# Kernel optimization log

Hardware: AMD Instinct MI355X
Metric: run time of the kernel (lower is better)

Reference implementation:

```python
import jax, jax.numpy as jnp
import numpy as np

V, E, H, L = 50257, 256, 1024, 2   # vocab, embed_dim, hidden_dim, num_layers
B, T, K = 64, 80, 5                # batch, max_len, top_k
TEMP = 0.75
TWO_PI_OVER_24 = np.float32(2.0 * np.pi / 24.0)


def setup_inputs() -> dict:
    key = jax.random.key(0)
    ks = jax.random.split(key, 12)
    n = lambda i, shape, s: (jax.random.normal(ks[i], shape, jnp.float32) * s)
    hours = jax.random.uniform(ks[0], (B,), jnp.float32) * 24.0
    return {
        "hours": hours,
        "tp_w1": n(1, (2, H), 0.5),
        "tp_b1": jnp.zeros((H,), jnp.float32),
        "tp_w2": n(2, (H, 2 * L * H), 0.02),
        "tp_b2": jnp.zeros((2 * L * H,), jnp.float32),
        "embed": n(3, (V, E), 0.1).at[0].set(0.0),  # padding_idx=0 row zeroed
        "w_ih0": n(4, (E, 4 * H), 0.05),
        "w_hh0": n(5, (H, 4 * H), 0.05),
        "b0": jnp.zeros((4 * H,), jnp.float32),     # b_ih + b_hh combined
        "w_ih1": n(6, (H, 4 * H), 0.05),
        "w_hh1": n(7, (H, 4 * H), 0.05),
        "b1": jnp.zeros((4 * H,), jnp.float32),
        "fc_w": n(8, (H, V), 0.02),
        "fc_b": jnp.zeros((V,), jnp.float32),
        "sos_id": 1,
    }


def _lstm_cell(x, h, c, w_ih, w_hh, b):
    # torch gate order: i, f, g, o
    g = x @ w_ih + h @ w_hh + b
    i, f, gg, o = jnp.split(g, 4, axis=-1)
    c2 = jax.nn.sigmoid(f) * c + jax.nn.sigmoid(i) * jnp.tanh(gg)
    h2 = jax.nn.sigmoid(o) * jnp.tanh(c2)
    return h2, c2


def reference(hours, tp_w1, tp_b1, tp_w2, tp_b2, embed,
              w_ih0, w_hh0, b0, w_ih1, w_hh1, b1, fc_w, fc_b, sos_id):
    # _encode_time: sin/cos of hour angle -> MLP -> (h0, c0) per layer
    a = hours * TWO_PI_OVER_24
    feat = jnp.stack([jnp.sin(a), jnp.cos(a)], axis=-1)          # [B,2]
    tp = jnp.tanh(feat @ tp_w1 + tp_b1) @ tp_w2 + tp_b2          # [B,2*L*H]
    tp = tp.reshape(B, L, 2, H)
    h = jnp.transpose(tp[:, :, 0, :], (1, 0, 2))                 # [L,B,H]
    c = jnp.transpose(tp[:, :, 1, :], (1, 0, 2))                 # [L,B,H]

    keys = jax.random.split(jax.random.key(42), T)

    def step(carry, k):
        h, c, tok = carry
        x = embed[tok]                                           # [B,E]
        h0n, c0n = _lstm_cell(x, h[0], c[0], w_ih0, w_hh0, b0)
        h1n, c1n = _lstm_cell(h0n, h[1], c[1], w_ih1, w_hh1, b1)
        logits = (h1n @ fc_w + fc_b) / TEMP                      # [B,V]
        topv, topi = jax.lax.top_k(logits, K)                    # [B,K]
        probs = jax.nn.softmax(topv, axis=-1)
        sel = jax.random.categorical(k, topv, axis=-1)           # [B], == multinomial(probs)
        nxt = jnp.take_along_axis(topi, sel[:, None], axis=1)[:, 0]
        return (jnp.stack([h0n, h1n]), jnp.stack([c0n, c1n]), nxt), (nxt, probs)

    tok0 = jnp.full((B,), sos_id, jnp.int32)
    _, (toks, probs) = jax.lax.scan(step, (h, c, tok0), keys)
    # toks: [T,B] -> [B,T]; probs: [T,B,K] -> [B,T,K]
    return jnp.transpose(toks, (1, 0)), jnp.transpose(probs, (1, 0, 2))
```

## Files before the change

### kernel.cpp

```cpp
#include <hip/hip_runtime.h>
#include <math.h>
#include <stdint.h>
#include <limits.h>

#define VSZ 50257
#define ESZ 256
#define HSZ 1024
#define BSZ 64
#define TSZ 80
#define GC  4096
#define NFCB 786
#define NCAND (NFCB*5)
#define NSLOT 26
#define NREF 12

typedef unsigned int u32;
typedef unsigned short u16;
typedef double f64x4 __attribute__((ext_vector_type(4)));
typedef float f32x4v __attribute__((ext_vector_type(4)));
typedef __bf16 bf16x8 __attribute__((ext_vector_type(8)));
union BFrag { u16 u[8]; bf16x8 v; };

__device__ __forceinline__ u16 f2bf(float f) {
  u32 x = __float_as_uint(f);
  return (u16)((x + 0x7FFFu + ((x >> 16) & 1u)) >> 16);
}
__device__ __forceinline__ float bf2f(u16 h) { return __uint_as_float(((u32)h) << 16); }

__device__ __forceinline__ void tf2x32(u32 k0, u32 k1, u32& x0, u32& x1) {
  u32 ks2 = k0 ^ k1 ^ 0x1BD11BDAu;
  x0 += k0; x1 += k1;
#define RND(r) { x0 += x1; x1 = (x1 << r) | (x1 >> (32 - r)); x1 ^= x0; }
  RND(13) RND(15) RND(26) RND(6)
  x0 += k1; x1 += ks2 + 1u;
  RND(17) RND(29) RND(16) RND(24)
  x0 += ks2; x1 += k0 + 2u;
  RND(13) RND(15) RND(26) RND(6)
  x0 += k0; x1 += k1 + 3u;
  RND(17) RND(29) RND(16) RND(24)
  x0 += k1; x1 += ks2 + 4u;
  RND(13) RND(15) RND(26) RND(6)
  x0 += ks2; x1 += k0 + 5u;
#undef RND
}

__device__ __forceinline__ double dsig(double x) { return 0.5 + 0.5 * tanh(0.5 * x); }

__device__ __forceinline__ void ins5(double v, int i, double* tv, int* ti) {
  bool beat4 = (v > tv[4]) || (v == tv[4] && i < ti[4]);
  if (!beat4) return;
  tv[4] = v; ti[4] = i;
#pragma unroll
  for (int p = 4; p > 0; --p) {
    bool sw = (tv[p] > tv[p-1]) || (tv[p] == tv[p-1] && ti[p] < ti[p-1]);
    double a0 = sw ? tv[p] : tv[p-1]; double a1 = sw ? tv[p-1] : tv[p];
    tv[p-1] = a0; tv[p] = a1;
    int b0 = sw ? ti[p] : ti[p-1]; int b1 = sw ? ti[p-1] : ti[p];
    ti[p-1] = b0; ti[p] = b1;
  }
}

__device__ __forceinline__ double dref(int m, int n) {
  int s = 0;
#pragma unroll
  for (int k = 0; k < 4; ++k) s += (4*m + k + 1) * (16*k + n + 1);
  return (double)s;
}

__global__ __launch_bounds__(64) void k_probe(int* __restrict__ fbp) {
  int l = threadIdx.x;
  int lane16 = l & 15, sub = l >> 4;
  {
    double av = (double)(4 * lane16 + sub + 1);
    double bv = (double)(16 * sub + lane16 + 1);
    f64x4 acc = {0., 0., 0., 0.};
    acc = __builtin_amdgcn_mfma_f64_16x16x4f64(av, bv, acc, 0, 0, 0);
    bool o0 = true, o1 = true, o2 = true, o3 = true;
#pragma unroll
    for (int j = 0; j < 4; ++j) {
      double d = acc[j];
      o0 = o0 && (d == dref(4 * sub + j, lane16));
      o1 = o1 && (d == dref(lane16, 4 * sub + j));
      o2 = o2 && (d == dref(sub + 4 * j, lane16));
      o3 = o3 && (d == dref(lane16, sub + 4 * j));
    }
    int a0 = __all(o0), a1 = __all(o1), a2 = __all(o2), a3 = __all(o3);
    if (l == 0) { fbp[0] = a0 ? 0 : a1 ? 1 : a2 ? 2 : 3; fbp[1] = 0; }
  }
  {
    BFrag fa, fbv;
#pragma unroll
    for (int i = 0; i < 8; ++i) {
      int k = sub * 8 + i;
      fa.u[i]  = f2bf((float)((lane16 * 5 + k * 3) % 63 + 1));
      fbv.u[i] = f2bf((float)((k * 7 + lane16 * 11) % 61 + 1));
    }
    f32x4v c = {0.f, 0.f, 0.f, 0.f};
    c = __builtin_amdgcn_mfma_f32_16x16x32_bf16(fa.v, fbv.v, c, 0, 0, 0);
    bool okb = true;
#pragma unroll
    for (int j = 0; j < 4; ++j) {
      int mm = sub * 4 + j, nn = lane16;
      int ref = 0;
      for (int k = 0; k < 32; ++k) ref += ((mm*5 + k*3) % 63 + 1) * ((k*7 + nn*11) % 61 + 1);
      okb = okb && (c[j] == (float)ref);
    }
    int allb = __all(okb);
    if (l == 0) fbp[2] = allb;
  }
}

__global__ __launch_bounds__(256) void k_rng(double* __restrict__ gum) {
  int idx = blockIdx.x * 256 + threadIdx.x;
  if (idx >= TSZ * 320) return;
  int t = idx / 320, m = idx % 320;
  u32 a0 = 0u, a1 = (u32)t;
  tf2x32(0u, 42u, a0, a1);
  u32 x0 = 0u, x1 = (u32)m;
  tf2x32(a0, a1, x0, x1);
  u32 bits = x0 ^ x1;
  const float TINY = 1.17549435082228750797e-38f;
  float f = __uint_as_float((bits >> 9) | 0x3f800000u) - 1.0f;
  float u = f + TINY;
  u = fmaxf(TINY, u);
  gum[idx] = -log(-log((double)u));
}

__global__ __launch_bounds__(256) void k_time1(const float* __restrict__ hours, const float* __restrict__ w1,
                                               const float* __restrict__ bb1, double* __restrict__ tp1T) {
  int idx = blockIdx.x * 256 + threadIdx.x;
  int b = idx & 63, hcol = idx >> 6;
  const float TPO = (float)(2.0 * 3.14159265358979323846 / 24.0);
  float af = hours[b] * TPO;
  double a = (double)af;
  double sv = sin(a), cv = cos(a);
  double vv = tanh(sv * (double)w1[hcol] + cv * (double)w1[HSZ + hcol] + (double)bb1[hcol]);
  tp1T[(size_t)hcol * 64 + b] = vv;
}

__global__ __launch_bounds__(256) void k_gemm_simple(const double* __restrict__ XTa, const float* __restrict__ Wa,
                                                     int Ka, int Sa, double* __restrict__ part) {
  int j = blockIdx.x * 256 + threadIdx.x;
  if (j >= GC) return;
  int s = blockIdx.y;
  int kc = Ka / Sa, k0 = s * kc;
  double acc[BSZ];
#pragma unroll
  for (int b = 0; b < BSZ; ++b) acc[b] = 0.0;
  const float* wp = Wa + (size_t)k0 * GC + j;
  const double* xp = XTa + (size_t)k0 * 64;
  for (int k = 0; k < kc; ++k) {
    double wv = (double)wp[0]; wp += GC;
#pragma unroll
    for (int b = 0; b < BSZ; ++b) acc[b] = fma(wv, xp[b], acc[b]);
    xp += 64;
  }
  double* o = part + ((size_t)s * 64) * GC + j;
#pragma unroll
  for (int b = 0; b < BSZ; ++b) o[(size_t)b * GC] = acc[b];
}

__global__ __launch_bounds__(256) void k_t2r(const double* __restrict__ part, const float* __restrict__ b2,
                                             double* __restrict__ h0T, double* __restrict__ c0,
                                             double* __restrict__ h1T, double* __restrict__ c1) {
  int b = blockIdx.y;
  int j = blockIdx.x * 256 + threadIdx.x;
  double acc = (double)b2[j];
  for (int s = 0; s < 8; ++s) acc += part[((size_t)s * 64 + b) * GC + j];
  int l = j >> 11, half = (j >> 10) & 1, hcol = j & 1023;
  if (half == 0) (l ? h1T : h0T)[(size_t)hcol * 64 + b] = acc;
  else           (l ? c1 : c0)[(size_t)b * HSZ + hcol] = acc;
}

__global__ __launch_bounds__(256, 4) void k_lstm_mfma(const double* __restrict__ x0, const float* __restrict__ W0,
                                                      const double* __restrict__ x1, const float* __restrict__ W1,
                                                      const double* __restrict__ x2, const float* __restrict__ W2,
                                                      int s1, int s2, double* __restrict__ part,
                                                      const int* __restrict__ fbp) {
  int conv = fbp[0] & 3;
  __shared__ double xs[64 * 64];
  int tid = threadIdx.x;
  int l = tid & 63, wv = tid >> 6;
  int sub = l >> 4, lane16 = l & 15;
  int colbase = blockIdx.x * 64;
  int s = blockIdx.y;
  const double* XT; const float* W; int k0;
  if (s < s1)      { XT = x0; W = W0; k0 = s * 128; }
  else if (s < s2) { XT = x1; W = W1; k0 = (s - s1) * 128; }
  else             { XT = x2; W = W2; k0 = (s - s2) * 128; }
  int colA = colbase + wv * 16 + lane16;
  f64x4 a0 = {0.,0.,0.,0.}, a1 = {0.,0.,0.,0.}, a2 = {0.,0.,0.,0.}, a3 = {0.,0.,0.,0.};
  const float* wp = W + (size_t)(k0 + sub) * GC + colA;
  float ab[8];
#pragma unroll
  for (int u = 0; u < 8; ++u) { ab[u] = wp[0]; wp += (size_t)4 * GC; }
  for (int ch = 0; ch < 2; ++ch) {
    __syncthreads();
    const double2* src = (const double2*)(XT + (size_t)(k0 + ch * 64) * 64);
    double2* dst = (double2*)xs;
    for (int i = tid; i < 2048; i += 256) dst[i] = src[i];
    __syncthreads();
#pragma unroll
    for (int g = 0; g < 2; ++g) {
#pragma unroll
      for (int u = 0; u < 8; ++u) {
        int ks = g * 8 + u;
        int step = ch * 16 + ks;
        float nv = 0.f;
        if (step + 8 < 32) nv = wp[0];
        wp += (size_t)4 * GC;
        double av = (double)ab[u];
        const double* bp = xs + (ks * 4 + sub) * 64 + lane16;
        double b0 = bp[0], b1 = bp[16], b2 = bp[32], b3 = bp[48];
        a0 = __builtin_amdgcn_mfma_f64_16x16x4f64(av, b0, a0, 0, 0, 0);
        a1 = __builtin_amdgcn_mfma_f64_16x16x4f64(av, b1, a1, 0, 0, 0);
        a2 = __builtin_amdgcn_mfma_f64_16x16x4f64(av, b2, a2, 0, 0, 0);
        a3 = __builtin_amdgcn_mfma_f64_16x16x4f64(av, b3, a3, 0, 0, 0);
        ab[u] = nv;
      }
    }
  }
#pragma unroll
  for (int j = 0; j < 4; ++j) {
    int m = (conv == 0) ? sub * 4 + j : (conv == 2) ? sub + 4 * j : lane16;
    int n = (conv == 0) ? lane16 : (conv == 2) ? lane16 : ((conv == 1) ? sub * 4 + j : sub + 4 * j);
    size_t base = ((size_t)s * 64 + n) * GC + colbase + wv * 16 + m;
    part[base]                   = a0[j];
    part[base + (size_t)16 * GC] = a1[j];
    part[base + (size_t)32 * GC] = a2[j];
    part[base + (size_t)48 * GC] = a3[j];
  }
}

__global__ __launch_bounds__(256) void k_cell(const double* __restrict__ part, int sBeg, int S,
                                              const float* __restrict__ bias,
                                              double* __restrict__ c, double* __restrict__ hT,
                                              int emit, u16* __restrict__ xh, u16* __restrict__ xl) {
  int b = blockIdx.y;
  int hcol = blockIdx.x * 256 + threadIdx.x;
  double gi = (double)bias[hcol];
  double gf = (double)bias[1024 + hcol];
  double gg = (double)bias[2048 + hcol];
  double go = (double)bias[3072 + hcol];
#pragma unroll 4
  for (int s = sBeg; s < sBeg + S; ++s) {
    const double* p = part + ((size_t)s * 64 + b) * GC;
    gi += p[hcol]; gf += p[1024 + hcol]; gg += p[2048 + hcol]; go += p[3072 + hcol];
  }
  size_t ci = (size_t)b * HSZ + hcol;
  double cn = dsig(gf) * c[ci] + dsig(gi) * tanh(gg);
  double hn = dsig(go) * tanh(cn);
  c[ci] = cn;
  hT[(size_t)hcol * 64 + b] = hn;
  if (emit) {
    u16 hb = f2bf((float)hn);
    double r = hn - (double)bf2f(hb);
    u16 lb = f2bf((float)r);
    size_t ti2 = (((size_t)(hcol >> 3)) * 64 + b) * 8 + (hcol & 7);
    xh[ti2] = hb;
    xl[ti2] = lb;
  }
}

__global__ __launch_bounds__(256, 4) void k_fcbf(const u16* __restrict__ xhg, const u16* __restrict__ xlg,
                                                 const float* __restrict__ W, const float* __restrict__ fcb,
                                                 double* __restrict__ candV, int* __restrict__ candI,
                                                 const int* __restrict__ fbp) {
  if (fbp[2] == 0) return;
  __shared__ double xs[64 * 64];
  u16* lx = (u16*)xs;
  int tid = threadIdx.x;
  int l = tid & 63, wv = tid >> 6;
  int sub = l >> 4, lane16 = l & 15;
  int vbase = blockIdx.x * 64;
  int colA = min(vbase + wv * 16 + lane16, VSZ - 1);
  f32x4v acc0 = {0,0,0,0}, acc1 = {0,0,0,0}, acc2 = {0,0,0,0}, acc3 = {0,0,0,0};
  for (int ch = 0; ch < 8; ++ch) {
    float wraw[32];
    const float* wb = W + (size_t)(ch * 128) * VSZ + colA;
#pragma unroll
    for (int q = 0; q < 32; ++q) {
      int k = ((q >> 3) * 32) + sub * 8 + (q & 7);
      wraw[q] = wb[(size_t)k * VSZ];
    }
    __syncthreads();
    {
      const uint4* sh = (const uint4*)(xhg + (size_t)ch * 8192);
      const uint4* sl = (const uint4*)(xlg + (size_t)ch * 8192);
      uint4* dh = (uint4*)lx;
      uint4* dl = (uint4*)(lx + 8192);
      for (int i = tid; i < 1024; i += 256) { dh[i] = sh[i]; dl[i] = sl[i]; }
    }
    __syncthreads();
#pragma unroll
    for (int kt = 0; kt < 4; ++kt) {
      BFrag wh, wl;
#pragma unroll
      for (int i = 0; i < 8; ++i) {
        float w = wraw[kt * 8 + i];
        u16 hb = f2bf(w);
        wh.u[i] = hb;
        wl.u[i] = f2bf(w - bf2f(hb));
      }
      int r = kt * 4 + sub;
#define BT_STEP(BT, ACC)                                                              \
      {                                                                               \
        int bb = BT * 16 + lane16;                                                    \
        bf16x8 xhv = *(const bf16x8*)(lx + (((size_t)r * 64 + bb) << 3));             \
        bf16x8 xlv = *(const bf16x8*)(lx + 8192 + (((size_t)r * 64 + bb) << 3));      \
        ACC = __builtin_amdgcn_mfma_f32_16x16x32_bf16(wh.v, xhv, ACC, 0, 0, 0);       \
        ACC = __builtin_amdgcn_mfma_f32_16x16x32_bf16(wh.v, xlv, ACC, 0, 0, 0);       \
        ACC = __builtin_amdgcn_mfma_f32_16x16x32_bf16(wl.v, xhv, ACC, 0, 0, 0);       \
      }
      BT_STEP(0, acc0)
      BT_STEP(1, acc1)
      BT_STEP(2, acc2)
      BT_STEP(3, acc3)
#undef BT_STEP
    }
  }
  __syncthreads();
#pragma unroll
  for (int j = 0; j < 4; ++j) {
    int vl = wv * 16 + sub * 4 + j;
    int v = vbase + vl;
    bool okv = (v < VSZ);
    double bi = okv ? (double)fcb[min(v, VSZ - 1)] : 0.0;
    int b0i = lane16, b1i = 16 + lane16, b2i = 32 + lane16, b3i = 48 + lane16;
    xs[b0i * 64 + ((vl + b0i) & 63)] = okv ? ((double)acc0[j] + bi) / 0.75 : -INFINITY;
    xs[b1i * 64 + ((vl + b1i) & 63)] = okv ? ((double)acc1[j] + bi) / 0.75 : -INFINITY;
    xs[b2i * 64 + ((vl + b2i) & 63)] = okv ? ((double)acc2[j] + bi) / 0.75 : -INFINITY;
    xs[b3i * 64 + ((vl + b3i) & 63)] = okv ? ((double)acc3[j] + bi) / 0.75 : -INFINITY;
  }
  __syncthreads();
  if (tid < 64) {
    int b = tid;
    double tv[5]; int ti[5];
#pragma unroll
    for (int p = 0; p < 5; ++p) { tv[p] = -INFINITY; ti[p] = INT_MAX; }
    for (int vl2 = 0; vl2 < 64; ++vl2)
      ins5(xs[b * 64 + ((vl2 + b) & 63)], vbase + vl2, tv, ti);
#pragma unroll
    for (int r = 0; r < 5; ++r) {
      candV[(size_t)b * NCAND + blockIdx.x * 5 + r] = tv[r];
      candI[(size_t)b * NCAND + blockIdx.x * 5 + r] = ti[r];
    }
  }
}

__global__ __launch_bounds__(256, 4) void k_fcf64(const double* __restrict__ h1T, const float* __restrict__ W,
                                                  const float* __restrict__ fcb,
                                                  double* __restrict__ candV, int* __restrict__ candI,
                                                  const int* __restrict__ fbp) {
  if (fbp[2] != 0) return;
  int conv = fbp[0] & 3;
  __shared__ double xs[64 * 64];
  int tid = threadIdx.x;
  int l = tid & 63, wv = tid >> 6;
  int sub = l >> 4, lane16 = l & 15;
  int vbase = blockIdx.x * 64;
  int colA = min(vbase + wv * 16 + lane16, VSZ - 1);
  f64x4 a0 = {0.,0.,0.,0.}, a1 = {0.,0.,0.,0.}, a2 = {0.,0.,0.,0.}, a3 = {0.,0.,0.,0.};
  const float* wp = W + (size_t)sub * VSZ + colA;
  float ab[8];
#pragma unroll
  for (int u = 0; u < 8; ++u) { ab[u] = wp[0]; wp += (size_t)4 * VSZ; }
  for (int ch = 0; ch < 16; ++ch) {
    __syncthreads();
    const double2* src = (const double2*)(h1T + (size_t)ch * 64 * 64);
    double2* dst = (double2*)xs;
    for (int i = tid; i < 2048; i += 256) dst[i] = src[i];
    __syncthreads();
#pragma unroll
    for (int g = 0; g < 2; ++g) {
#pragma unroll
      for (int u = 0; u < 8; ++u) {
        int ks = g * 8 + u;
        int step = ch * 16 + ks;
        float nv = 0.f;
        if (step + 8 < 256) nv = wp[0];
        wp += (size_t)4 * VSZ;
        double av = (double)ab[u];
        const double* bp = xs + (ks * 4 + sub) * 64 + lane16;
        double b0 = bp[0], b1 = bp[16], b2 = bp[32], b3 = bp[48];
        a0 = __builtin_amdgcn_mfma_f64_16x16x4f64(av, b0, a0, 0, 0, 0);
        a1 = __builtin_amdgcn_mfma_f64_16x16x4f64(av, b1, a1, 0, 0, 0);
        a2 = __builtin_amdgcn_mfma_f64_16x16x4f64(av, b2, a2, 0, 0, 0);
        a3 = __builtin_amdgcn_mfma_f64_16x16x4f64(av, b3, a3, 0, 0, 0);
        ab[u] = nv;
      }
    }
  }
  __syncthreads();
#pragma unroll
  for (int j = 0; j < 4; ++j) {
    int m = (conv == 0) ? sub * 4 + j : (conv == 2) ? sub + 4 * j : lane16;
    int n = (conv == 0) ? lane16 : (conv == 2) ? lane16 : ((conv == 1) ? sub * 4 + j : sub + 4 * j);
    int vl = wv * 16 + m;
    int v = vbase + vl;
    bool okv = (v < VSZ);
    double bi = okv ? (double)fcb[min(v, VSZ - 1)] : 0.0;
    int b0i = n, b1i = 16 + n, b2i = 32 + n, b3i = 48 + n;
    xs[b0i * 64 + ((vl + b0i) & 63)] = okv ? (a0[j] + bi) / 0.75 : -INFINITY;
    xs[b1i * 64 + ((vl + b1i) & 63)] = okv ? (a1[j] + bi) / 0.75 : -INFINITY;
    xs[b2i * 64 + ((vl + b2i) & 63)] = okv ? (a2[j] + bi) / 0.75 : -INFINITY;
    xs[b3i * 64 + ((vl + b3i) & 63)] = okv ? (a3[j] + bi) / 0.75 : -INFINITY;
  }
  __syncthreads();
  if (tid < 64) {
    int b = tid;
    double tv[5]; int ti[5];
#pragma unroll
    for (int p = 0; p < 5; ++p) { tv[p] = -INFINITY; ti[p] = INT_MAX; }
    for (int vl2 = 0; vl2 < 64; ++vl2)
      ins5(xs[b * 64 + ((vl2 + b) & 63)], vbase + vl2, tv, ti);
#pragma unroll
    for (int r = 0; r < 5; ++r) {
      candV[(size_t)b * NCAND + blockIdx.x * 5 + r] = tv[r];
      candI[(size_t)b * NCAND + blockIdx.x * 5 + r] = ti[r];
    }
  }
}

__global__ __launch_bounds__(256) void k_rfin(const double* __restrict__ candV, const int* __restrict__ candI,
                                              const float* __restrict__ W, const float* __restrict__ fcb,
                                              const double* __restrict__ h1T,
                                              const double* __restrict__ gum, int t,
                                              const float* __restrict__ embed,
                                              float* __restrict__ out, double* __restrict__ xt0) {
  __shared__ float sv[NCAND];
  __shared__ int   si[NCAND];
  __shared__ double redw[4];
  __shared__ float wvv[4]; __shared__ int wvi[4]; __shared__ int wvs[4];
  int b = blockIdx.x, tid = threadIdx.x;
  int l = tid & 63, wvd = tid >> 6;
  for (int e = tid; e < NCAND; e += 256) {
    sv[e] = (float)candV[(size_t)b * NCAND + e];
    si[e] = candI[(size_t)b * NCAND + e];
  }
  __syncthreads();
  int cidx[NREF];
#pragma unroll
  for (int r = 0; r < NREF; ++r) {
    float bv = -INFINITY; int bi = INT_MAX, bs = 0;
    for (int e = tid; e < NCAND; e += 256) {
      float v = sv[e]; int i2 = si[e];
      if (v > bv || (v == bv && i2 < bi)) { bv = v; bi = i2; bs = e; }
    }
#pragma unroll
    for (int off = 1; off < 64; off <<= 1) {
      float ov = __shfl_xor(bv, off, 64);
      int oi = __shfl_xor(bi, off, 64);
      int os = __shfl_xor(bs, off, 64);
      if (ov > bv || (ov == bv && oi < bi)) { bv = ov; bi = oi; bs = os; }
    }
    if (l == 0) { wvv[wvd] = bv; wvi[wvd] = bi; wvs[wvd] = bs; }
    __syncthreads();
    float fv = wvv[0]; int fi = wvi[0], fs = wvs[0];
#pragma unroll
    for (int q = 1; q < 4; ++q) {
      float ov = wvv[q]; int oi = wvi[q], os = wvs[q];
      if (ov > fv || (ov == fv && oi < fi)) { fv = ov; fi = oi; fs = os; }
    }
    cidx[r] = fi;
    __syncthreads();
    if (tid == 0) sv[fs] = -INFINITY;
    __syncthreads();
  }
  double ex[NREF];
#pragma unroll
  for (int c = 0; c < NREF; ++c) {
    int vc = cidx[c];
    double p = 0.0;
    for (int k = tid; k < HSZ; k += 256)
      p = fma((double)W[(size_t)k * VSZ + vc], h1T[(size_t)k * 64 + b], p);
#pragma unroll
    for (int off = 1; off < 64; off <<= 1) p += __shfl_xor(p, off, 64);
    if (l == 0) redw[wvd] = p;
    __syncthreads();
    ex[c] = ((redw[0] + redw[1] + redw[2] + redw[3]) + (double)fcb[vc]) / 0.75;
    __syncthreads();
  }
  double tv[5]; int ti[5];
#pragma unroll
  for (int p = 0; p < 5; ++p) { tv[p] = -INFINITY; ti[p] = INT_MAX; }
#pragma unroll
  for (int c = 0; c < NREF; ++c) ins5(ex[c], cidx[c], tv, ti);
  const double* g = gum + (size_t)t * 320 + b * 5;
  double bestv = tv[0] + g[0]; int best = 0;
#pragma unroll
  for (int k2 = 1; k2 < 5; ++k2) { double vv2 = tv[k2] + g[k2]; if (vv2 > bestv) { bestv = vv2; best = k2; } }
  int nxt = ti[best];
  if (tid == 0) {
    out[b * TSZ + t] = (float)nxt;
    double m = tv[0];
    double exx[5]; double s = 0.0;
#pragma unroll
    for (int k2 = 0; k2 < 5; ++k2) { exx[k2] = exp(tv[k2] - m); s += exx[k2]; }
    float* po = out + BSZ * TSZ + ((size_t)b * TSZ + t) * 5;
#pragma unroll
    for (int k2 = 0; k2 < 5; ++k2) po[k2] = (float)(exx[k2] / s);
  }
  xt0[(size_t)tid * 64 + b] = (double)embed[(size_t)nxt * ESZ + tid];
}

__global__ __launch_bounds__(256) void k_emb0(const float* __restrict__ embed, const int* __restrict__ sos,
                                              double* __restrict__ xt0) {
  int idx = blockIdx.x * 256 + threadIdx.x;
  int b = idx & 63, k = idx >> 6;
  xt0[(size_t)k * 64 + b] = (double)embed[(size_t)sos[0] * ESZ + k];
}

extern "C" void kernel_launch(void* const* d_in, const int* in_sizes, int n_in,
                              void* d_out, int out_size, void* d_ws, size_t ws_size,
                              hipStream_t stream) {
  const float* hours = (const float*)d_in[0];
  const float* tp_w1 = (const float*)d_in[1];
  const float* tp_b1 = (const float*)d_in[2];
  const float* tp_w2 = (const float*)d_in[3];
  const float* tp_b2 = (const float*)d_in[4];
  const float* embed = (const float*)d_in[5];
  const float* w_ih0 = (const float*)d_in[6];
  const float* w_hh0 = (const float*)d_in[7];
  const float* b0    = (const float*)d_in[8];
  const float* w_ih1 = (const float*)d_in[9];
  const float* w_hh1 = (const float*)d_in[10];
  const float* b1    = (const float*)d_in[11];
  const float* fc_w  = (const float*)d_in[12];
  const float* fc_b  = (const float*)d_in[13];
  const int*   sos   = (const int*)d_in[14];
  float* out = (float*)d_out;

  char* w = (char*)d_ws;
  double* part = (double*)w;  w += (size_t)NSLOT * 64 * GC * 8;
  double* xt0  = (double*)w;  w += (size_t)ESZ * 64 * 8;
  double* h0T  = (double*)w;  w += (size_t)HSZ * 64 * 8;
  double* h1T  = (double*)w;  w += (size_t)HSZ * 64 * 8;
  double* c0   = (double*)w;  w += (size_t)BSZ * HSZ * 8;
  double* c1   = (double*)w;  w += (size_t)BSZ * HSZ * 8;
  double* tp1T = (double*)w;  w += (size_t)HSZ * 64 * 8;
  double* gum  = (double*)w;  w += (size_t)TSZ * 320 * 8;
  double* candV = (double*)w; w += (size_t)BSZ * NCAND * 8;
  int*    candI = (int*)w;    w += (size_t)BSZ * NCAND * 4;
  int*    fbuf  = (int*)w;    w += 64;
  u16*    xhg   = (u16*)w;    w += (size_t)HSZ * 64 * 2;
  u16*    xlg   = (u16*)w;    w += (size_t)HSZ * 64 * 2;

  k_probe<<<dim3(1), dim3(64), 0, stream>>>(fbuf);
  k_rng<<<dim3(100), dim3(256), 0, stream>>>(gum);
  k_time1<<<dim3(256), dim3(256), 0, stream>>>(hours, tp_w1, tp_b1, tp1T);
  k_gemm_simple<<<dim3(16, 8), dim3(256), 0, stream>>>(tp1T, tp_w2, 1024, 8, part);
  k_t2r<<<dim3(16, 64), dim3(256), 0, stream>>>(part, tp_b2, h0T, c0, h1T, c1);
  k_emb0<<<dim3(64), dim3(256), 0, stream>>>(embed, sos, xt0);

  double* part18 = part + (size_t)18 * 64 * GC;
  for (int t = 0; t < TSZ; ++t) {
    k_lstm_mfma<<<dim3(64, 18), dim3(256), 0, stream>>>(xt0, w_ih0, h0T, w_hh0, h1T, w_hh1, 2, 10, part, fbuf);
    k_cell<<<dim3(4, 64), dim3(256), 0, stream>>>(part, 0, 10, b0, c0, h0T, 0, xhg, xlg);
    k_lstm_mfma<<<dim3(64, 8), dim3(256), 0, stream>>>(h0T, w_ih1, h0T, w_ih1, h0T, w_ih1, 8, 8, part18, fbuf);
    k_cell<<<dim3(4, 64), dim3(256), 0, stream>>>(part, 10, 16, b1, c1, h1T, 1, xhg, xlg);
    k_fcbf<<<dim3(NFCB), dim3(256), 0, stream>>>(xhg, xlg, fc_w, fc_b, candV, candI, fbuf);
    k_fcf64<<<dim3(NFCB), dim3(256), 0, stream>>>(h1T, fc_w, fc_b, candV, candI, fbuf);
    k_rfin<<<dim3(64), dim3(256), 0, stream>>>(candV, candI, fc_w, fc_b, h1T, gum, t, embed, out, xt0);
  }
}
```

Before: 20.50 ms.

## Pre-convert FC weights to transposed bf16 and drop split-bf16 candidate pass

Converts the fc weight matrix once per call into a transposed bf16 copy, so the per-step candidate GEMM loads contiguous bf16 rows and issues one MFMA per tile instead of three (hi/lo split). It also swizzles the shared-memory layout of the hidden state. The LSTM split-K slices grow from 128 to 256, which halves the partial-sum slots and launched blocks, and the top-candidate refinement count rises to 16 with one warp per candidate and no per-candidate barriers. This trades candidate accuracy for speed, covered by the larger exact-fp64 refinement set, and needs about 100MB of extra workspace, falling back to the fp64 path when that is not available.

```diff
diff --git a/kernel.cpp b/kernel.cpp
--- a/kernel.cpp
+++ b/kernel.cpp
@@ -11,8 +11,8 @@
 #define GC  4096
 #define NFCB 786
 #define NCAND (NFCB*5)
-#define NSLOT 26
-#define NREF 12
+#define NSLOT 13
+#define NREF 16
 
 typedef unsigned int u32;
 typedef unsigned short u16;
@@ -110,6 +110,25 @@
   }
 }
 
+__global__ __launch_bounds__(256) void k_wconv(const float* __restrict__ W, u16* __restrict__ whT) {
+  __shared__ u16 tile[64][65];
+  int vb = blockIdx.x * 64, kb = blockIdx.y * 64;
+  int tid = threadIdx.x;
+#pragma unroll
+  for (int i = 0; i < 16; ++i) {
+    int r = i * 4 + (tid >> 6), c = tid & 63;
+    int v = vb + c;
+    tile[c][r] = (v < VSZ) ? f2bf(W[(size_t)(kb + r) * VSZ + v]) : (u16)0;
+  }
+  __syncthreads();
+#pragma unroll
+  for (int i = 0; i < 16; ++i) {
+    int r = i * 4 + (tid >> 6), c = tid & 63;
+    int v = vb + r;
+    if (v < VSZ) whT[(size_t)v * 1024 + kb + c] = tile[r][c];
+  }
+}
+
 __global__ __launch_bounds__(256) void k_rng(double* __restrict__ gum) {
   int idx = blockIdx.x * 256 + threadIdx.x;
   if (idx >= TSZ * 320) return;
@@ -185,16 +204,16 @@
   int colbase = blockIdx.x * 64;
   int s = blockIdx.y;
   const double* XT; const float* W; int k0;
-  if (s < s1)      { XT = x0; W = W0; k0 = s * 128; }
-  else if (s < s2) { XT = x1; W = W1; k0 = (s - s1) * 128; }
-  else             { XT = x2; W = W2; k0 = (s - s2) * 128; }
+  if (s < s1)      { XT = x0; W = W0; k0 = s * 256; }
+  else if (s < s2) { XT = x1; W = W1; k0 = (s - s1) * 256; }
+  else             { XT = x2; W = W2; k0 = (s - s2) * 256; }
   int colA = colbase + wv * 16 + lane16;
   f64x4 a0 = {0.,0.,0.,0.}, a1 = {0.,0.,0.,0.}, a2 = {0.,0.,0.,0.}, a3 = {0.,0.,0.,0.};
   const float* wp = W + (size_t)(k0 + sub) * GC + colA;
   float ab[8];
 #pragma unroll
   for (int u = 0; u < 8; ++u) { ab[u] = wp[0]; wp += (size_t)4 * GC; }
-  for (int ch = 0; ch < 2; ++ch) {
+  for (int ch = 0; ch < 4; ++ch) {
     __syncthreads();
     const double2* src = (const double2*)(XT + (size_t)(k0 + ch * 64) * 64);
     double2* dst = (double2*)xs;
@@ -207,7 +226,7 @@
         int ks = g * 8 + u;
         int step = ch * 16 + ks;
         float nv = 0.f;
-        if (step + 8 < 32) nv = wp[0];
+        if (step + 8 < 64) nv = wp[0];
         wp += (size_t)4 * GC;
         double av = (double)ab[u];
         const double* bp = xs + (ks * 4 + sub) * 64 + lane16;
@@ -235,7 +254,7 @@
 __global__ __launch_bounds__(256) void k_cell(const double* __restrict__ part, int sBeg, int S,
                                               const float* __restrict__ bias,
                                               double* __restrict__ c, double* __restrict__ hT,
-                                              int emit, u16* __restrict__ xh, u16* __restrict__ xl) {
+                                              int emit, u16* __restrict__ xh) {
   int b = blockIdx.y;
   int hcol = blockIdx.x * 256 + threadIdx.x;
   double gi = (double)bias[hcol];
@@ -252,18 +271,12 @@
   double hn = dsig(go) * tanh(cn);
   c[ci] = cn;
   hT[(size_t)hcol * 64 + b] = hn;
-  if (emit) {
-    u16 hb = f2bf((float)hn);
-    double r = hn - (double)bf2f(hb);
-    u16 lb = f2bf((float)r);
-    size_t ti2 = (((size_t)(hcol >> 3)) * 64 + b) * 8 + (hcol & 7);
-    xh[ti2] = hb;
-    xl[ti2] = lb;
-  }
-}
-
-__global__ __launch_bounds__(256, 4) void k_fcbf(const u16* __restrict__ xhg, const u16* __restrict__ xlg,
-                                                 const float* __restrict__ W, const float* __restrict__ fcb,
+  if (emit)
+    xh[(size_t)(hcol >> 7) * 8192 + (size_t)b * 128 + (hcol & 127)] = f2bf((float)hn);
+}
+
+__global__ __launch_bounds__(256, 4) void k_fcbf(const u16* __restrict__ xhg, const u16* __restrict__ whT,
+                                                 const float* __restrict__ fcb,
                                                  double* __restrict__ candV, int* __restrict__ candI,
                                                  const int* __restrict__ fbp) {
   if (fbp[2] == 0) return;
@@ -274,44 +287,32 @@
   int sub = l >> 4, lane16 = l & 15;
   int vbase = blockIdx.x * 64;
   int colA = min(vbase + wv * 16 + lane16, VSZ - 1);
+  const u16* wrow = whT + (size_t)colA * 1024;
   f32x4v acc0 = {0,0,0,0}, acc1 = {0,0,0,0}, acc2 = {0,0,0,0}, acc3 = {0,0,0,0};
   for (int ch = 0; ch < 8; ++ch) {
-    float wraw[32];
-    const float* wb = W + (size_t)(ch * 128) * VSZ + colA;
-#pragma unroll
-    for (int q = 0; q < 32; ++q) {
-      int k = ((q >> 3) * 32) + sub * 8 + (q & 7);
-      wraw[q] = wb[(size_t)k * VSZ];
-    }
+    bf16x8 wh0 = *(const bf16x8*)(wrow + ch * 128 + 0 * 32 + sub * 8);
+    bf16x8 wh1 = *(const bf16x8*)(wrow + ch * 128 + 1 * 32 + sub * 8);
+    bf16x8 wh2 = *(const bf16x8*)(wrow + ch * 128 + 2 * 32 + sub * 8);
+    bf16x8 wh3 = *(const bf16x8*)(wrow + ch * 128 + 3 * 32 + sub * 8);
     __syncthreads();
     {
-      const uint4* sh = (const uint4*)(xhg + (size_t)ch * 8192);
-      const uint4* sl = (const uint4*)(xlg + (size_t)ch * 8192);
-      uint4* dh = (uint4*)lx;
-      uint4* dl = (uint4*)(lx + 8192);
-      for (int i = tid; i < 1024; i += 256) { dh[i] = sh[i]; dl[i] = sl[i]; }
+      const uint4* sg = (const uint4*)(xhg + (size_t)ch * 8192);
+      uint4* dl = (uint4*)lx;
+#pragma unroll
+      for (int i = 0; i < 4; ++i) {
+        int u = tid + i * 256;
+        int bswz = u >> 4, g = u & 15;
+        dl[(bswz << 4) | (g ^ (bswz & 7))] = sg[u];
+      }
     }
     __syncthreads();
 #pragma unroll
     for (int kt = 0; kt < 4; ++kt) {
-      BFrag wh, wl;
-#pragma unroll
-      for (int i = 0; i < 8; ++i) {
-        float w = wraw[kt * 8 + i];
-        u16 hb = f2bf(w);
-        wh.u[i] = hb;
-        wl.u[i] = f2bf(w - bf2f(hb));
-      }
-      int r = kt * 4 + sub;
-#define BT_STEP(BT, ACC)                                                              \
-      {                                                                               \
-        int bb = BT * 16 + lane16;                                                    \
-        bf16x8 xhv = *(const bf16x8*)(lx + (((size_t)r * 64 + bb) << 3));             \
-        bf16x8 xlv = *(const bf16x8*)(lx + 8192 + (((size_t)r * 64 + bb) << 3));      \
-        ACC = __builtin_amdgcn_mfma_f32_16x16x32_bf16(wh.v, xhv, ACC, 0, 0, 0);       \
-        ACC = __builtin_amdgcn_mfma_f32_16x16x32_bf16(wh.v, xlv, ACC, 0, 0, 0);       \
-        ACC = __builtin_amdgcn_mfma_f32_16x16x32_bf16(wl.v, xhv, ACC, 0, 0, 0);       \
-      }
+      bf16x8 whv = (kt == 0) ? wh0 : (kt == 1) ? wh1 : (kt == 2) ? wh2 : wh3;
+#define BT_STEP(BT, ACC) {                                                              \
+        int bb = BT * 16 + lane16;                                                      \
+        const bf16x8* bp2 = (const bf16x8*)lx + ((bb << 4) | ((kt * 4 + sub) ^ (bb & 7))); \
+        ACC = __builtin_amdgcn_mfma_f32_16x16x32_bf16(whv, *bp2, ACC, 0, 0, 0); }
       BT_STEP(0, acc0)
       BT_STEP(1, acc1)
       BT_STEP(2, acc2)
@@ -351,8 +352,8 @@
 __global__ __launch_bounds__(256, 4) void k_fcf64(const double* __restrict__ h1T, const float* __restrict__ W,
                                                   const float* __restrict__ fcb,
                                                   double* __restrict__ candV, int* __restrict__ candI,
-                                                  const int* __restrict__ fbp) {
-  if (fbp[2] != 0) return;
+                                                  const int* __restrict__ fbp, int force) {
+  if (!force && fbp[2] != 0) return;
   int conv = fbp[0] & 3;
   __shared__ double xs[64 * 64];
   int tid = threadIdx.x;
@@ -430,7 +431,7 @@
                                               float* __restrict__ out, double* __restrict__ xt0) {
   __shared__ float sv[NCAND];
   __shared__ int   si[NCAND];
-  __shared__ double redw[4];
+  __shared__ double exS[NREF];
   __shared__ float wvv[4]; __shared__ int wvi[4]; __shared__ int wvs[4];
   int b = blockIdx.x, tid = threadIdx.x;
   int l = tid & 63, wvd = tid >> 6;
@@ -467,25 +468,26 @@
     if (tid == 0) sv[fs] = -INFINITY;
     __syncthreads();
   }
-  double ex[NREF];
-#pragma unroll
-  for (int c = 0; c < NREF; ++c) {
+#pragma unroll
+  for (int rr = 0; rr < 4; ++rr) {
+    int c = wvd + rr * 4;
     int vc = cidx[c];
     double p = 0.0;
-    for (int k = tid; k < HSZ; k += 256)
+#pragma unroll
+    for (int i = 0; i < 16; ++i) {
+      int k = i * 64 + l;
       p = fma((double)W[(size_t)k * VSZ + vc], h1T[(size_t)k * 64 + b], p);
+    }
 #pragma unroll
     for (int off = 1; off < 64; off <<= 1) p += __shfl_xor(p, off, 64);
-    if (l == 0) redw[wvd] = p;
-    __syncthreads();
-    ex[c] = ((redw[0] + redw[1] + redw[2] + redw[3]) + (double)fcb[vc]) / 0.75;
-    __syncthreads();
-  }
+    if (l == 0) exS[c] = (p + (double)fcb[vc]) / 0.75;
+  }
+  __syncthreads();
   double tv[5]; int ti[5];
 #pragma unroll
   for (int p = 0; p < 5; ++p) { tv[p] = -INFINITY; ti[p] = INT_MAX; }
 #pragma unroll
-  for (int c = 0; c < NREF; ++c) ins5(ex[c], cidx[c], tv, ti);
+  for (int c = 0; c < NREF; ++c) ins5(exS[c], cidx[c], tv, ti);
   const double* g = gum + (size_t)t * 320 + b * 5;
   double bestv = tv[0] + g[0]; int best = 0;
 #pragma unroll
@@ -544,7 +546,9 @@
   int*    candI = (int*)w;    w += (size_t)BSZ * NCAND * 4;
   int*    fbuf  = (int*)w;    w += 64;
   u16*    xhg   = (u16*)w;    w += (size_t)HSZ * 64 * 2;
-  u16*    xlg   = (u16*)w;    w += (size_t)HSZ * 64 * 2;
+  u16*    whT   = (u16*)w;    w += (size_t)VSZ * 1024 * 2;
+  size_t need = (size_t)(w - (char*)d_ws);
+  int useBF = (ws_size >= need) ? 1 : 0;
 
   k_probe<<<dim3(1), dim3(64), 0, stream>>>(fbuf);
   k_rng<<<dim3(100), dim3(256), 0, stream>>>(gum);
@@ -552,15 +556,18 @@
   k_gemm_simple<<<dim3(16, 8), dim3(256), 0, stream>>>(tp1T, tp_w2, 1024, 8, part);
   k_t2r<<<dim3(16, 64), dim3(256), 0, stream>>>(part, tp_b2, h0T, c0, h1T, c1);
   k_emb0<<<dim3(64), dim3(256), 0, stream>>>(embed, sos, xt0);
-
-  double* part18 = part + (size_t)18 * 64 * GC;
+  if (useBF)
+    k_wconv<<<dim3(786, 16), dim3(256), 0, stream>>>(fc_w, whT);
+
+  double* part9 = part + (size_t)9 * 64 * GC;
   for (int t = 0; t < TSZ; ++t) {
-    k_lstm_mfma<<<dim3(64, 18), dim3(256), 0, stream>>>(xt0, w_ih0, h0T, w_hh0, h1T, w_hh1, 2, 10, part, fbuf);
-    k_cell<<<dim3(4, 64), dim3(256), 0, stream>>>(part, 0, 10, b0, c0, h0T, 0, xhg, xlg);
-    k_lstm_mfma<<<dim3(64, 8), dim3(256), 0, stream>>>(h0T, w_ih1, h0T, w_ih1, h0T, w_ih1, 8, 8, part18, fbuf);
-    k_cell<<<dim3(4, 64), dim3(256), 0, stream>>>(part, 10, 16, b1, c1, h1T, 1, xhg, xlg);
-    k_fcbf<<<dim3(NFCB), dim3(256), 0, stream>>>(xhg, xlg, fc_w, fc_b, candV, candI, fbuf);
-    k_fcf64<<<dim3(NFCB), dim3(256), 0, stream>>>(h1T, fc_w, fc_b, candV, candI, fbuf);
+    k_lstm_mfma<<<dim3(64, 9), dim3(256), 0, stream>>>(xt0, w_ih0, h0T, w_hh0, h1T, w_hh1, 1, 5, part, fbuf);
+    k_cell<<<dim3(4, 64), dim3(256), 0, stream>>>(part, 0, 5, b0, c0, h0T, 0, xhg);
+    k_lstm_mfma<<<dim3(64, 4), dim3(256), 0, stream>>>(h0T, w_ih1, h0T, w_ih1, h0T, w_ih1, 4, 4, part9, fbuf);
+    k_cell<<<dim3(4, 64), dim3(256), 0, stream>>>(part, 5, 8, b1, c1, h1T, 1, xhg);
+    if (useBF)
+      k_fcbf<<<dim3(NFCB), dim3(256), 0, stream>>>(xhg, whT, fc_b, candV, candI, fbuf);
+    k_fcf64<<<dim3(NFCB), dim3(256), 0, stream>>>(h1T, fc_w, fc_b, candV, candI, fbuf, useBF ? 0 : 1);
     k_rfin<<<dim3(64), dim3(256), 0, stream>>>(candV, candI, fc_w, fc_b, h1T, gum, t, embed, out, xt0);
   }
 }
```

Measured after the change: 19.11 ms. 6.7% less time.
